# Performance work log

Hardware: AMD Instinct MI355X
Metric: run time of the kernel (lower is better)

## Reference

```python
import jax, jax.numpy as jnp
import numpy as np

IMG = 640
C = 80
K = 10
LB, LC = 7.5, 0.5
ALPHA_COST, BETA_COST = 0.5, 6.0
GAMMA, ALPHA = 2.0, 0.25
EPS = 1e-7
PI = 3.141592653589793


def xywh_to_xyxy(b):
    cx, cy, w, h = b[..., 0], b[..., 1], b[..., 2], b[..., 3]
    return jnp.stack([cx - w * 0.5, cy - h * 0.5, cx + w * 0.5, cy + h * 0.5], axis=-1)


def bbox_iou(box1, box2):
    # box1 [M,4], box2 [N,4] xyxy -> [M,N]
    area1 = jnp.clip(box1[:, 2] - box1[:, 0], 0) * jnp.clip(box1[:, 3] - box1[:, 1], 0)
    area2 = jnp.clip(box2[:, 2] - box2[:, 0], 0) * jnp.clip(box2[:, 3] - box2[:, 1], 0)
    ix1 = jnp.maximum(box1[:, None, 0], box2[None, :, 0])
    iy1 = jnp.maximum(box1[:, None, 1], box2[None, :, 1])
    ix2 = jnp.minimum(box1[:, None, 2], box2[None, :, 2])
    iy2 = jnp.minimum(box1[:, None, 3], box2[None, :, 3])
    inter = jnp.clip(ix2 - ix1, 0) * jnp.clip(iy2 - iy1, 0)
    union = area1[:, None] + area2[None, :] - inter + EPS
    return jnp.clip(inter / union, 0.0, 1.0)


def bbox_ciou(p, t):
    # elementwise [N,4] x [N,4] xyxy -> [N]
    px1, py1, px2, py2 = p[:, 0], p[:, 1], p[:, 2], p[:, 3]
    tx1, ty1, tx2, ty2 = t[:, 0], t[:, 1], t[:, 2], t[:, 3]
    pw = jnp.clip(px2 - px1, EPS)
    ph = jnp.clip(py2 - py1, EPS)
    tw = jnp.clip(tx2 - tx1, EPS)
    th = jnp.clip(ty2 - ty1, EPS)
    inter = jnp.clip(jnp.minimum(px2, tx2) - jnp.maximum(px1, tx1), 0) * \
            jnp.clip(jnp.minimum(py2, ty2) - jnp.maximum(py1, ty1), 0)
    union = pw * ph + tw * th - inter + EPS
    iou = inter / union
    cd = ((px1 + px2) * 0.5 - (tx1 + tx2) * 0.5) ** 2 + ((py1 + py2) * 0.5 - (ty1 + ty2) * 0.5) ** 2
    cw = jnp.maximum(px2, tx2) - jnp.minimum(px1, tx1)
    ch = jnp.maximum(py2, ty2) - jnp.minimum(py1, ty1)
    c2 = cw ** 2 + ch ** 2 + EPS
    v = (4.0 / PI ** 2) * (jnp.arctan(tw / th) - jnp.arctan(pw / ph)) ** 2
    alpha = jax.lax.stop_gradient(v / (v - iou + 1.0 + EPS))
    return iou - cd / c2 - alpha * v


def _decode(p, stride):
    # p: [B, A, S, S, E] -> box [B, A*S*S, 4] (xywh px), cls [B, A*S*S, C]
    B, A, S, _, E = p.shape
    tx, ty, tw, th = p[..., 0], p[..., 1], p[..., 2], p[..., 3]
    gy, gx = jnp.meshgrid(jnp.arange(S, dtype=p.dtype), jnp.arange(S, dtype=p.dtype), indexing='ij')
    gx = gx.reshape(1, 1, S, S)
    gy = gy.reshape(1, 1, S, S)
    px = (jax.nn.sigmoid(tx) * 2.0 - 0.5 + gx) * stride  # center_mode='v8'
    py = (jax.nn.sigmoid(ty) * 2.0 - 0.5 + gy) * stride
    pw = jax.nn.softplus(tw) * stride                      # wh_mode='softplus'
    ph = jax.nn.softplus(th) * stride
    box = jnp.stack([px, py, pw, ph], axis=-1).reshape(B, -1, 4)
    cls = p[..., 4:].reshape(B, -1, C)
    return box, cls


def _per_image(p_box, p_logits, gt, labels):
    # p_box [M,4] xywh, p_logits [M,C], gt [N,4] xyxy, labels [N]
    N = gt.shape[0]
    tcx = (gt[:, 0] + gt[:, 2]) * 0.5
    tcy = (gt[:, 1] + gt[:, 3]) * 0.5
    dist = (p_box[:, 0][:, None] - tcx[None, :]) ** 2 + (p_box[:, 1][:, None] - tcy[None, :]) ** 2  # [M,N]
    _, cand = jax.lax.top_k(-dist.T, K)       # [N,K] nearest anchors per target
    cand = cand.reshape(-1)                    # [N*K] (dups don't change the min)
    cand_box = p_box[cand]
    cand_logits = p_logits[cand]
    cls_score = jax.nn.sigmoid(cand_logits)[:, labels]          # [NK,N]
    iou = bbox_iou(xywh_to_xyxy(cand_box), gt)                  # [NK,N]
    cost = ALPHA_COST * (1.0 - cls_score) + BETA_COST * (1.0 - iou)
    matched = cand[jnp.argmin(cost, axis=0)]                    # [N]
    ciou = bbox_ciou(xywh_to_xyxy(p_box[matched]), gt)
    loss_box = LB * jnp.sum(1.0 - ciou) / N
    tgt = jnp.zeros_like(p_logits).at[matched, labels].set(1.0)  # [M,C]
    x = p_logits
    ce = jnp.maximum(x, 0) - x * tgt + jnp.log1p(jnp.exp(-jnp.abs(x)))
    pr = jax.nn.sigmoid(x)
    p_t = pr * tgt + (1 - pr) * (1 - tgt)
    fl = ce * (1 - p_t) ** GAMMA
    a_t = ALPHA * tgt + (1 - ALPHA) * (1 - tgt)
    loss_cls = LC * jnp.sum(a_t * fl) / N
    return loss_box + loss_cls


def _forward(p0, p1, p2, gt_boxes, labels):
    boxes, logits = [], []
    for p in (p0, p1, p2):
        S = p.shape[2]
        pb, pl = _decode(p, float(IMG) / S)
        boxes.append(pb)
        logits.append(pl)
    flat_boxes = jnp.concatenate(boxes, axis=1)    # [B, 8400, 4]
    flat_logits = jnp.concatenate(logits, axis=1)  # [B, 8400, C]
    per_img = jax.vmap(_per_image)(flat_boxes, flat_logits, gt_boxes, labels)  # [B]
    return jnp.mean(per_img)


def setup_inputs() -> dict:
    key = jax.random.key(0)
    k0, k1, k2, kc, kw, kl = jax.random.split(key, 6)
    B, N = 16, 60
    p0 = jax.random.normal(k0, (B, 1, 80, 80, 84), dtype=jnp.float32)
    p1 = jax.random.normal(k1, (B, 1, 40, 40, 84), dtype=jnp.float32)
    p2 = jax.random.normal(k2, (B, 1, 20, 20, 84), dtype=jnp.float32)
    c = jax.random.uniform(kc, (B, N, 2), minval=64.0, maxval=576.0)
    wh = jax.random.uniform(kw, (B, N, 2), minval=8.0, maxval=128.0)
    gt_boxes = jnp.concatenate([c - wh * 0.5, c + wh * 0.5], axis=-1).astype(jnp.float32)
    labels = jax.random.randint(kl, (B, N), 0, 80, dtype=jnp.int32)
    return {"p0": p0, "p1": p1, "p2": p2, "gt_boxes": gt_boxes, "labels": labels}


def reference(p0, p1, p2, gt_boxes, labels):
    return _forward(p0, p1, p2, gt_boxes, labels)
```

## Files before the change

kernel.cpp:

```cpp
#include <hip/hip_runtime.h>
#include <cfloat>
#include <math.h>

#define NB   16
#define NGT  60
#define NA   8400
#define KNN  10
#define NCAND (NGT*KNN)
#define EPSF 1e-7f
#define PIF  3.14159265358979f
#define FOCAL_BLOCKS 2048

#define LOG2E 1.44269504088896341f
#define LN2   0.69314718055994531f

__device__ __forceinline__ float fexp2(float x){ return __builtin_amdgcn_exp2f(x); }
__device__ __forceinline__ float flog2(float x){ return __builtin_amdgcn_logf(x); }
__device__ __forceinline__ float frcp (float x){ return __builtin_amdgcn_rcpf(x); }

__device__ __forceinline__ float fsigm(float x){
  return frcp(1.0f + fexp2(-x*LOG2E));
}
__device__ __forceinline__ float fsoftplus(float x){
  float u = fexp2(-fabsf(x)*LOG2E);
  return fmaxf(x,0.f) + LN2*flog2(1.0f + u);
}
__device__ __forceinline__ float fbg(float x){
  float u = fexp2(fminf(-x*LOG2E, 126.0f));
  float t = frcp(1.0f + u);
  return (x + LN2*flog2(1.0f + u)) * t * t;
}

template<int S, int BASE, int STRIDE_I>
__device__ __forceinline__ void do_vec(const float* __restrict__ p, unsigned vloc,
                                       float4* __restrict__ boxes, float& sum){
  unsigned s = vloc*4u;
  float4 x4 = *(const float4*)(p + s);
  if ((s % 84u) == 0u){
    unsigned row   = s / 84u;
    unsigned img   = row / (unsigned)(S*S);
    unsigned local = row - img*(unsigned)(S*S);
    unsigned i = local / (unsigned)S, j = local - i*(unsigned)S;
    const float stf = (float)STRIDE_I;
    float px = (fsigm(x4.x)*2.f - 0.5f + (float)j)*stf;
    float py = (fsigm(x4.y)*2.f - 0.5f + (float)i)*stf;
    float pw = fsoftplus(x4.z)*stf;
    float ph = fsoftplus(x4.w)*stf;
    boxes[(size_t)img*NA + BASE + local] = make_float4(px,py,pw,ph);
  } else {
    sum += fbg(x4.x) + fbg(x4.y) + fbg(x4.z) + fbg(x4.w);
  }
}

__global__ __launch_bounds__(256) void fused_decode_focal(const float* __restrict__ p0,
                                                          const float* __restrict__ p1,
                                                          const float* __restrict__ p2,
                                                          float4* __restrict__ boxes,
                                                          float* __restrict__ fsum){
  const unsigned nv0 = NB*6400u*84u/4u;
  const unsigned nv1 = NB*1600u*84u/4u;
  const unsigned nv2 = NB*400u*84u/4u;
  const unsigned total = nv0+nv1+nv2;
  __shared__ float sbuf[4];
  float sum = 0.f;
  unsigned stride = gridDim.x*blockDim.x;
  for (unsigned v = blockIdx.x*blockDim.x + threadIdx.x; v < total; v += stride){
    if (v < nv0)          do_vec<80,    0,  8>(p0, v,          boxes, sum);
    else if (v < nv0+nv1) do_vec<40, 6400, 16>(p1, v-nv0,      boxes, sum);
    else                  do_vec<20, 8000, 32>(p2, v-nv0-nv1,  boxes, sum);
  }
  sum *= 0.75f;
  #pragma unroll
  for (int off=32; off>0; off>>=1) sum += __shfl_xor(sum, off);
  int wid = threadIdx.x >> 6;
  if ((threadIdx.x & 63) == 0) sbuf[wid] = sum;
  __syncthreads();
  if (threadIdx.x == 0) fsum[blockIdx.x] = sbuf[0]+sbuf[1]+sbuf[2]+sbuf[3];
}

__device__ __forceinline__ const float* anchor_base(const float* p0,const float* p1,const float* p2,int img,int a){
  if (a < 6400) return p0 + (size_t)(img*6400 + a)*84;
  if (a < 8000) return p1 + (size_t)(img*1600 + (a-6400))*84;
  return p2 + (size_t)(img*400 + (a-8000))*84;
}

__global__ __launch_bounds__(256) void topk_kernel(const float4* __restrict__ boxes,
                                                   const float* __restrict__ gt,
                                                   int* __restrict__ cand){
  int wid  = threadIdx.x >> 6;
  int lane = threadIdx.x & 63;
  int pair = blockIdx.x*4 + wid;
  int img = pair / NGT, g = pair - img*NGT;
  const float* gb = gt + (size_t)(img*NGT + g)*4;
  float tcx = (gb[0]+gb[2])*0.5f, tcy = (gb[1]+gb[3])*0.5f;

  int jx0 = (int)(tcx * 0.125f),   iy0 = (int)(tcy * 0.125f);
  int jx1 = (int)(tcx * 0.0625f),  iy1 = (int)(tcy * 0.0625f);
  int jx2 = (int)(tcx * 0.03125f), iy2 = (int)(tcy * 0.03125f);

  const float4* bb = boxes + (size_t)img*NA;

  float d0=FLT_MAX,d1=FLT_MAX,d2=FLT_MAX,d3=FLT_MAX;
  int   a0,a1,a2,a3;
  #pragma unroll
  for (int s=0; s<4; s++){
    int c = lane + 64*s;
    float dd = FLT_MAX; int aa = 9000000 + c;
    int i, j, S, base, valid = 1;
    if (c < 169)      { int r=c/13,  q=c-13*r;           i=iy0-6+r; j=jx0-6+q; S=80; base=0; }
    else if (c < 218) { int t=c-169; int r=t/7, q=t-7*r; i=iy1-3+r; j=jx1-3+q; S=40; base=6400; }
    else if (c < 243) { int t=c-218; int r=t/5, q=t-5*r; i=iy2-2+r; j=jx2-2+q; S=20; base=8000; }
    else { valid = 0; i=j=0; S=1; base=0; }
    if (valid && i>=0 && i<S && j>=0 && j<S){
      int anchor = base + i*S + j;
      float4 b = bb[anchor];
      float dx=b.x-tcx, dy=b.y-tcy;
      dd = dx*dx + dy*dy;
      aa = anchor;
    }
    if (s==0){ d0=dd; a0=aa; } else if (s==1){ d1=dd; a1=aa; }
    else if (s==2){ d2=dd; a2=aa; } else { d3=dd; a3=aa; }
  }

  for (int r=0; r<KNN; r++){
    float v = d0; int anc = a0;
    if (d1 < v || (d1==v && a1<anc)){ v=d1; anc=a1; }
    if (d2 < v || (d2==v && a2<anc)){ v=d2; anc=a2; }
    if (d3 < v || (d3==v && a3<anc)){ v=d3; anc=a3; }
    #pragma unroll
    for (int off=32; off>0; off>>=1){
      float v2 = __shfl_xor(v, off);
      int  A2 = __shfl_xor(anc, off);
      if (v2 < v || (v2==v && A2<anc)){ v=v2; anc=A2; }
    }
    if (a0==anc) d0=FLT_MAX;
    if (a1==anc) d1=FLT_MAX;
    if (a2==anc) d2=FLT_MAX;
    if (a3==anc) d3=FLT_MAX;
    if (lane == 0) cand[(size_t)pair*KNN + r] = anc;
  }
}

__global__ __launch_bounds__(256) void match_kernel(const float4* __restrict__ boxes,
                                                    const int* __restrict__ cand,
                                                    const float* __restrict__ gt,
                                                    const int* __restrict__ labels,
                                                    const float* __restrict__ p0,
                                                    const float* __restrict__ p1,
                                                    const float* __restrict__ p2,
                                                    int* __restrict__ matched){
  int pair = blockIdx.x;
  int img = pair / NGT, j = pair - img*NGT;
  int tid = threadIdx.x;
  int wid = tid >> 6, lane = tid & 63;
  const float* gb = gt + (size_t)(img*NGT + j)*4;
  float gx=gb[0], gy=gb[1], gz=gb[2], gw=gb[3];
  float a2 = fmaxf(gz-gx,0.f)*fmaxf(gw-gy,0.f);
  int lab = labels[img*NGT + j];

  const int* ci = cand + (size_t)img*NCAND;
  float best = FLT_MAX; int bslot = 1<<30; int banchor = -1;
  for (int c=tid; c<NCAND; c+=256){
    int a = ci[c];
    float4 b = boxes[(size_t)img*NA + a];
    float bx1=b.x-b.z*0.5f, by1=b.y-b.w*0.5f, bx2=b.x+b.z*0.5f, by2=b.y+b.w*0.5f;
    float a1 = fmaxf(bx2-bx1,0.f)*fmaxf(by2-by1,0.f);
    float ix1=fmaxf(bx1,gx), iy1=fmaxf(by1,gy);
    float ix2=fminf(bx2,gz), iy2=fminf(by2,gw);
    float inter = fmaxf(ix2-ix1,0.f)*fmaxf(iy2-iy1,0.f);
    float uni = a1 + a2 - inter + EPSF;
    float iou = fminf(fmaxf(inter/uni,0.f),1.f);
    float lg = anchor_base(p0,p1,p2,img,a)[4+lab];
    float cost = 0.5f*(1.f - fsigm(lg)) + 6.f*(1.f - iou);
    if (cost < best){ best=cost; bslot=c; banchor=a; }
  }
  #pragma unroll
  for (int off=32; off>0; off>>=1){
    float v2 = __shfl_xor(best, off);
    int  s2 = __shfl_xor(bslot, off);
    int  a2s= __shfl_xor(banchor, off);
    if (v2 < best || (v2==best && s2<bslot)){ best=v2; bslot=s2; banchor=a2s; }
  }
  __shared__ float bc[4]; __shared__ int bs[4], ba[4];
  if (lane == 0){ bc[wid]=best; bs[wid]=bslot; ba[wid]=banchor; }
  __syncthreads();
  if (tid == 0){
    float v=bc[0]; int s=bs[0]; int a=ba[0];
    #pragma unroll
    for (int k=1;k<4;k++){
      if (bc[k] < v || (bc[k]==v && bs[k]<s)){ v=bc[k]; s=bs[k]; a=ba[k]; }
    }
    matched[img*NGT + j] = a;
  }
}

__global__ __launch_bounds__(1024) void tail_kernel(const float4* __restrict__ boxes,
                                                    const int* __restrict__ matched_g,
                                                    const float* __restrict__ gt,
                                                    const int* __restrict__ labels,
                                                    const float* __restrict__ p0,
                                                    const float* __restrict__ p1,
                                                    const float* __restrict__ p2,
                                                    const float* __restrict__ fsum,
                                                    float* __restrict__ out){
  int tid = threadIdx.x;
  int wid = tid >> 6;
  int lane = tid & 63;
  __shared__ int sm[NB][NGT];
  __shared__ int sl[NB][NGT];
  __shared__ float wb[NB], wc[NB], wf[NB];
  if (lane < NGT){
    sm[wid][lane] = matched_g[wid*NGT + lane];
    sl[wid][lane] = labels[wid*NGT + lane];
  }
  __syncthreads();

  int img = wid;
  float local_box = 0.f, local_corr = 0.f;
  if (lane < NGT){
    int j = lane;
    int m = sm[img][j];
    float4 pb = boxes[(size_t)img*NA + m];
    float px1=pb.x-pb.z*0.5f, py1=pb.y-pb.w*0.5f, px2=pb.x+pb.z*0.5f, py2=pb.y+pb.w*0.5f;
    const float* gb = gt + (size_t)(img*NGT + j)*4;
    float gx=gb[0], gy=gb[1], gz=gb[2], gw=gb[3];
    float pw=fmaxf(px2-px1,EPSF), ph=fmaxf(py2-py1,EPSF);
    float tw=fmaxf(gz-gx,EPSF),  th=fmaxf(gw-gy,EPSF);
    float inter = fmaxf(fminf(px2,gz)-fmaxf(px1,gx),0.f)*fmaxf(fminf(py2,gw)-fmaxf(py1,gy),0.f);
    float uni = pw*ph + tw*th - inter + EPSF;
    float iou = inter/uni;
    float dcx = (px1+px2)*0.5f - (gx+gz)*0.5f;
    float dcy = (py1+py2)*0.5f - (gy+gw)*0.5f;
    float cd = dcx*dcx + dcy*dcy;
    float cw = fmaxf(px2,gz) - fminf(px1,gx);
    float ch = fmaxf(py2,gw) - fminf(py1,gy);
    float c2 = cw*cw + ch*ch + EPSF;
    float dv = atanf(tw/th) - atanf(pw/ph);
    float v  = (4.f/(PIF*PIF))*dv*dv;
    float alpha = v/(v - iou + 1.f + EPSF);
    float ciou = iou - cd/c2 - alpha*v;
    local_box = 1.f - ciou;

    int lab = sl[img][j];
    bool dup = false;
    for (int j2=0; j2<j; j2++)
      if (sm[img][j2]==m && sl[img][j2]==lab){ dup=true; break; }
    if (!dup){
      float x = anchor_base(p0,p1,p2,img,m)[4+lab];
      float s  = fsigm(x);
      float u  = fexp2(-fabsf(x)*LOG2E);
      float lt = LN2*flog2(1.0f + u);
      float sp_pos = fmaxf(-x,0.f) + lt;
      float sp_neg = fmaxf( x,0.f) + lt;
      local_corr = 0.25f*sp_pos*(1.f-s)*(1.f-s) - 0.75f*sp_neg*s*s;
    }
  }
  float local_f = fsum[tid] + fsum[tid + 1024];
  #pragma unroll
  for (int off=32; off>0; off>>=1){
    local_box  += __shfl_xor(local_box,  off);
    local_corr += __shfl_xor(local_corr, off);
    local_f    += __shfl_xor(local_f,    off);
  }
  if (lane == 0){ wb[wid]=local_box; wc[wid]=local_corr; wf[wid]=local_f; }
  __syncthreads();
  if (tid == 0){
    float sb=0.f, sc=0.f, sf=0.f;
    #pragma unroll
    for (int k=0;k<NB;k++){ sb+=wb[k]; sc+=wc[k]; sf+=wf[k]; }
    out[0] = (7.5f*sb + 0.5f*(sf + sc)) / (60.f*16.f);
  }
}

extern "C" void kernel_launch(void* const* d_in, const int* in_sizes, int n_in,
                              void* d_out, int out_size, void* d_ws, size_t ws_size,
                              hipStream_t stream){
  const float* p0 = (const float*)d_in[0];
  const float* p1 = (const float*)d_in[1];
  const float* p2 = (const float*)d_in[2];
  const float* gt = (const float*)d_in[3];
  const int* labels = (const int*)d_in[4];
  float* out = (float*)d_out;

  float4* boxes   = (float4*)d_ws;
  int*    cand    = (int*)((char*)d_ws + (size_t)NB*NA*sizeof(float4));
  int*    matched = (int*)((char*)cand + (size_t)NB*NCAND*sizeof(int));
  float*  fsum    = (float*)((char*)matched + (size_t)NB*NGT*sizeof(int));

  fused_decode_focal<<<FOCAL_BLOCKS, 256, 0, stream>>>(p0, p1, p2, boxes, fsum);
  topk_kernel<<<NB*NGT/4, 256, 0, stream>>>(boxes, gt, cand);
  match_kernel<<<NB*NGT, 256, 0, stream>>>(boxes, cand, gt, labels, p0, p1, p2, matched);
  tail_kernel<<<1, 1024, 0, stream>>>(boxes, matched, gt, labels, p0, p1, p2, fsum, out);
}
```

Measured before the change: 47.68 us.

## Fuse match and tail kernels via last-block atomic; split focal vs decode work

Merges the match kernel and the single-block tail kernel into one launch, where the last block to finish (detected by an atomic counter reset in the decode kernel) performs the final CIoU/correction/focal reduction. Also reorganizes the decode/focal loop so focal-only float4 vectors are enumerated directly (skipping the box columns) and box rows are decoded in a separate index range, removing the per-vector modulo branch divergence. This removes one kernel launch and the divergent branch, at the cost of an atomic plus threadfence per block and a serialized tail on one 256-thread block.

```diff
diff --git a/kernel.cpp b/kernel.cpp
--- a/kernel.cpp
+++ b/kernel.cpp
@@ -11,6 +11,13 @@
 #define PIF  3.14159265358979f
 #define FOCAL_BLOCKS 2048
 
+#define NV0   2150400u
+#define NV1    537600u
+#define NV2    134400u
+#define NVTOT 2822400u
+#define NROWS  134400u
+#define FOCAL_COUNT 2688000u
+
 #define LOG2E 1.44269504088896341f
 #define LN2   0.69314718055994531f
 
@@ -32,42 +39,46 @@
 }
 
 template<int S, int BASE, int STRIDE_I>
-__device__ __forceinline__ void do_vec(const float* __restrict__ p, unsigned vloc,
-                                       float4* __restrict__ boxes, float& sum){
-  unsigned s = vloc*4u;
-  float4 x4 = *(const float4*)(p + s);
-  if ((s % 84u) == 0u){
-    unsigned row   = s / 84u;
-    unsigned img   = row / (unsigned)(S*S);
-    unsigned local = row - img*(unsigned)(S*S);
-    unsigned i = local / (unsigned)S, j = local - i*(unsigned)S;
-    const float stf = (float)STRIDE_I;
-    float px = (fsigm(x4.x)*2.f - 0.5f + (float)j)*stf;
-    float py = (fsigm(x4.y)*2.f - 0.5f + (float)i)*stf;
-    float pw = fsoftplus(x4.z)*stf;
-    float ph = fsoftplus(x4.w)*stf;
-    boxes[(size_t)img*NA + BASE + local] = make_float4(px,py,pw,ph);
-  } else {
-    sum += fbg(x4.x) + fbg(x4.y) + fbg(x4.z) + fbg(x4.w);
-  }
+__device__ __forceinline__ void decode_row(const float* __restrict__ p, unsigned row,
+                                           float4* __restrict__ boxes){
+  unsigned img   = row / (unsigned)(S*S);
+  unsigned local = row - img*(unsigned)(S*S);
+  unsigned i = local / (unsigned)S, j = local - i*(unsigned)S;
+  float4 x4 = *(const float4*)(p + (size_t)row*84u);
+  const float stf = (float)STRIDE_I;
+  float px = (fsigm(x4.x)*2.f - 0.5f + (float)j)*stf;
+  float py = (fsigm(x4.y)*2.f - 0.5f + (float)i)*stf;
+  float pw = fsoftplus(x4.z)*stf;
+  float ph = fsoftplus(x4.w)*stf;
+  boxes[(size_t)img*NA + BASE + local] = make_float4(px,py,pw,ph);
 }
 
 __global__ __launch_bounds__(256) void fused_decode_focal(const float* __restrict__ p0,
                                                           const float* __restrict__ p1,
                                                           const float* __restrict__ p2,
                                                           float4* __restrict__ boxes,
-                                                          float* __restrict__ fsum){
-  const unsigned nv0 = NB*6400u*84u/4u;
-  const unsigned nv1 = NB*1600u*84u/4u;
-  const unsigned nv2 = NB*400u*84u/4u;
-  const unsigned total = nv0+nv1+nv2;
+                                                          float* __restrict__ fsum,
+                                                          int* __restrict__ done){
+  if (blockIdx.x == 0 && threadIdx.x == 0) *done = 0;
   __shared__ float sbuf[4];
   float sum = 0.f;
   unsigned stride = gridDim.x*blockDim.x;
-  for (unsigned v = blockIdx.x*blockDim.x + threadIdx.x; v < total; v += stride){
-    if (v < nv0)          do_vec<80,    0,  8>(p0, v,          boxes, sum);
-    else if (v < nv0+nv1) do_vec<40, 6400, 16>(p1, v-nv0,      boxes, sum);
-    else                  do_vec<20, 8000, 32>(p2, v-nv0-nv1,  boxes, sum);
+  for (unsigned u = blockIdx.x*blockDim.x + threadIdx.x; u < NVTOT; u += stride){
+    if (u < FOCAL_COUNT){
+      unsigned g = u / 20u;
+      unsigned v = 21u*g + (u - 20u*g) + 1u;
+      const float* p; unsigned vloc;
+      if (v < NV0)           { p=p0; vloc = v; }
+      else if (v < NV0+NV1)  { p=p1; vloc = v - NV0; }
+      else                   { p=p2; vloc = v - (NV0+NV1); }
+      float4 x4 = *(const float4*)(p + (size_t)vloc*4u);
+      sum += fbg(x4.x) + fbg(x4.y) + fbg(x4.z) + fbg(x4.w);
+    } else {
+      unsigned row = u - FOCAL_COUNT;
+      if (row < 102400u)      decode_row<80,    0,  8>(p0, row,           boxes);
+      else if (row < 128000u) decode_row<40, 6400, 16>(p1, row - 102400u, boxes);
+      else                    decode_row<20, 8000, 32>(p2, row - 128000u, boxes);
+    }
   }
   sum *= 0.75f;
   #pragma unroll
@@ -141,133 +152,138 @@
   }
 }
 
-__global__ __launch_bounds__(256) void match_kernel(const float4* __restrict__ boxes,
-                                                    const int* __restrict__ cand,
-                                                    const float* __restrict__ gt,
-                                                    const int* __restrict__ labels,
-                                                    const float* __restrict__ p0,
-                                                    const float* __restrict__ p1,
-                                                    const float* __restrict__ p2,
-                                                    int* __restrict__ matched){
+__global__ __launch_bounds__(256) void match_tail_kernel(const float4* __restrict__ boxes,
+                                                         const int* __restrict__ cand,
+                                                         const float* __restrict__ gt,
+                                                         const int* __restrict__ labels,
+                                                         const float* __restrict__ p0,
+                                                         const float* __restrict__ p1,
+                                                         const float* __restrict__ p2,
+                                                         int* __restrict__ matched,
+                                                         const float* __restrict__ fsum,
+                                                         int* __restrict__ done,
+                                                         float* __restrict__ out){
   int pair = blockIdx.x;
   int img = pair / NGT, j = pair - img*NGT;
   int tid = threadIdx.x;
   int wid = tid >> 6, lane = tid & 63;
-  const float* gb = gt + (size_t)(img*NGT + j)*4;
-  float gx=gb[0], gy=gb[1], gz=gb[2], gw=gb[3];
-  float a2 = fmaxf(gz-gx,0.f)*fmaxf(gw-gy,0.f);
-  int lab = labels[img*NGT + j];
-
-  const int* ci = cand + (size_t)img*NCAND;
-  float best = FLT_MAX; int bslot = 1<<30; int banchor = -1;
-  for (int c=tid; c<NCAND; c+=256){
-    int a = ci[c];
-    float4 b = boxes[(size_t)img*NA + a];
-    float bx1=b.x-b.z*0.5f, by1=b.y-b.w*0.5f, bx2=b.x+b.z*0.5f, by2=b.y+b.w*0.5f;
-    float a1 = fmaxf(bx2-bx1,0.f)*fmaxf(by2-by1,0.f);
-    float ix1=fmaxf(bx1,gx), iy1=fmaxf(by1,gy);
-    float ix2=fminf(bx2,gz), iy2=fminf(by2,gw);
-    float inter = fmaxf(ix2-ix1,0.f)*fmaxf(iy2-iy1,0.f);
-    float uni = a1 + a2 - inter + EPSF;
-    float iou = fminf(fmaxf(inter/uni,0.f),1.f);
-    float lg = anchor_base(p0,p1,p2,img,a)[4+lab];
-    float cost = 0.5f*(1.f - fsigm(lg)) + 6.f*(1.f - iou);
-    if (cost < best){ best=cost; bslot=c; banchor=a; }
-  }
-  #pragma unroll
-  for (int off=32; off>0; off>>=1){
-    float v2 = __shfl_xor(best, off);
-    int  s2 = __shfl_xor(bslot, off);
-    int  a2s= __shfl_xor(banchor, off);
-    if (v2 < best || (v2==best && s2<bslot)){ best=v2; bslot=s2; banchor=a2s; }
-  }
-  __shared__ float bc[4]; __shared__ int bs[4], ba[4];
-  if (lane == 0){ bc[wid]=best; bs[wid]=bslot; ba[wid]=banchor; }
-  __syncthreads();
-  if (tid == 0){
-    float v=bc[0]; int s=bs[0]; int a=ba[0];
-    #pragma unroll
-    for (int k=1;k<4;k++){
-      if (bc[k] < v || (bc[k]==v && bs[k]<s)){ v=bc[k]; s=bs[k]; a=ba[k]; }
-    }
-    matched[img*NGT + j] = a;
-  }
-}
-
-__global__ __launch_bounds__(1024) void tail_kernel(const float4* __restrict__ boxes,
-                                                    const int* __restrict__ matched_g,
-                                                    const float* __restrict__ gt,
-                                                    const int* __restrict__ labels,
-                                                    const float* __restrict__ p0,
-                                                    const float* __restrict__ p1,
-                                                    const float* __restrict__ p2,
-                                                    const float* __restrict__ fsum,
-                                                    float* __restrict__ out){
-  int tid = threadIdx.x;
-  int wid = tid >> 6;
-  int lane = tid & 63;
-  __shared__ int sm[NB][NGT];
-  __shared__ int sl[NB][NGT];
-  __shared__ float wb[NB], wc[NB], wf[NB];
-  if (lane < NGT){
-    sm[wid][lane] = matched_g[wid*NGT + lane];
-    sl[wid][lane] = labels[wid*NGT + lane];
-  }
-  __syncthreads();
-
-  int img = wid;
-  float local_box = 0.f, local_corr = 0.f;
-  if (lane < NGT){
-    int j = lane;
-    int m = sm[img][j];
-    float4 pb = boxes[(size_t)img*NA + m];
-    float px1=pb.x-pb.z*0.5f, py1=pb.y-pb.w*0.5f, px2=pb.x+pb.z*0.5f, py2=pb.y+pb.w*0.5f;
+  {
     const float* gb = gt + (size_t)(img*NGT + j)*4;
     float gx=gb[0], gy=gb[1], gz=gb[2], gw=gb[3];
-    float pw=fmaxf(px2-px1,EPSF), ph=fmaxf(py2-py1,EPSF);
-    float tw=fmaxf(gz-gx,EPSF),  th=fmaxf(gw-gy,EPSF);
-    float inter = fmaxf(fminf(px2,gz)-fmaxf(px1,gx),0.f)*fmaxf(fminf(py2,gw)-fmaxf(py1,gy),0.f);
-    float uni = pw*ph + tw*th - inter + EPSF;
-    float iou = inter/uni;
-    float dcx = (px1+px2)*0.5f - (gx+gz)*0.5f;
-    float dcy = (py1+py2)*0.5f - (gy+gw)*0.5f;
-    float cd = dcx*dcx + dcy*dcy;
-    float cw = fmaxf(px2,gz) - fminf(px1,gx);
-    float ch = fmaxf(py2,gw) - fminf(py1,gy);
-    float c2 = cw*cw + ch*ch + EPSF;
-    float dv = atanf(tw/th) - atanf(pw/ph);
-    float v  = (4.f/(PIF*PIF))*dv*dv;
-    float alpha = v/(v - iou + 1.f + EPSF);
-    float ciou = iou - cd/c2 - alpha*v;
-    local_box = 1.f - ciou;
-
-    int lab = sl[img][j];
-    bool dup = false;
-    for (int j2=0; j2<j; j2++)
-      if (sm[img][j2]==m && sl[img][j2]==lab){ dup=true; break; }
-    if (!dup){
-      float x = anchor_base(p0,p1,p2,img,m)[4+lab];
-      float s  = fsigm(x);
-      float u  = fexp2(-fabsf(x)*LOG2E);
-      float lt = LN2*flog2(1.0f + u);
-      float sp_pos = fmaxf(-x,0.f) + lt;
-      float sp_neg = fmaxf( x,0.f) + lt;
-      local_corr = 0.25f*sp_pos*(1.f-s)*(1.f-s) - 0.75f*sp_neg*s*s;
-    }
-  }
-  float local_f = fsum[tid] + fsum[tid + 1024];
+    float a2 = fmaxf(gz-gx,0.f)*fmaxf(gw-gy,0.f);
+    int lab = labels[img*NGT + j];
+
+    const int* ci = cand + (size_t)img*NCAND;
+    float best = FLT_MAX; int bslot = 1<<30; int banchor = -1;
+    for (int c=tid; c<NCAND; c+=256){
+      int a = ci[c];
+      float4 b = boxes[(size_t)img*NA + a];
+      float bx1=b.x-b.z*0.5f, by1=b.y-b.w*0.5f, bx2=b.x+b.z*0.5f, by2=b.y+b.w*0.5f;
+      float a1 = fmaxf(bx2-bx1,0.f)*fmaxf(by2-by1,0.f);
+      float ix1=fmaxf(bx1,gx), iy1=fmaxf(by1,gy);
+      float ix2=fminf(bx2,gz), iy2=fminf(by2,gw);
+      float inter = fmaxf(ix2-ix1,0.f)*fmaxf(iy2-iy1,0.f);
+      float uni = a1 + a2 - inter + EPSF;
+      float iou = fminf(fmaxf(inter/uni,0.f),1.f);
+      float lg = anchor_base(p0,p1,p2,img,a)[4+lab];
+      float cost = 0.5f*(1.f - fsigm(lg)) + 6.f*(1.f - iou);
+      if (cost < best){ best=cost; bslot=c; banchor=a; }
+    }
+    #pragma unroll
+    for (int off=32; off>0; off>>=1){
+      float v2 = __shfl_xor(best, off);
+      int  s2 = __shfl_xor(bslot, off);
+      int  a2s= __shfl_xor(banchor, off);
+      if (v2 < best || (v2==best && s2<bslot)){ best=v2; bslot=s2; banchor=a2s; }
+    }
+    __shared__ float bc[4]; __shared__ int bs[4], ba[4];
+    if (lane == 0){ bc[wid]=best; bs[wid]=bslot; ba[wid]=banchor; }
+    __syncthreads();
+    if (tid == 0){
+      float v=bc[0]; int s=bs[0]; int a=ba[0];
+      #pragma unroll
+      for (int k=1;k<4;k++){
+        if (bc[k] < v || (bc[k]==v && bs[k]<s)){ v=bc[k]; s=bs[k]; a=ba[k]; }
+      }
+      matched[img*NGT + j] = a;
+    }
+  }
+
+  __shared__ int lastflag;
+  if (tid == 0){
+    __threadfence();
+    int old = atomicAdd(done, 1);
+    lastflag = (old == NB*NGT - 1);
+  }
+  __syncthreads();
+  if (!lastflag) return;
+  __threadfence();
+
+  __shared__ int sm[NB*NGT];
+  __shared__ int sl[NB*NGT];
+  for (int t=tid; t<NB*NGT; t+=256){ sm[t]=matched[t]; sl[t]=labels[t]; }
+  __syncthreads();
+
+  float local_box = 0.f, local_corr = 0.f;
+  #pragma unroll
+  for (int q=0; q<4; q++){
+    int im = wid*4 + q;
+    if (lane < NGT){
+      int jj = lane;
+      int m = sm[im*NGT + jj];
+      float4 pb = boxes[(size_t)im*NA + m];
+      float px1=pb.x-pb.z*0.5f, py1=pb.y-pb.w*0.5f, px2=pb.x+pb.z*0.5f, py2=pb.y+pb.w*0.5f;
+      const float* gb = gt + (size_t)(im*NGT + jj)*4;
+      float gx=gb[0], gy=gb[1], gz=gb[2], gw=gb[3];
+      float pw=fmaxf(px2-px1,EPSF), ph=fmaxf(py2-py1,EPSF);
+      float tw=fmaxf(gz-gx,EPSF),  th=fmaxf(gw-gy,EPSF);
+      float inter = fmaxf(fminf(px2,gz)-fmaxf(px1,gx),0.f)*fmaxf(fminf(py2,gw)-fmaxf(py1,gy),0.f);
+      float uni = pw*ph + tw*th - inter + EPSF;
+      float iou = inter/uni;
+      float dcx = (px1+px2)*0.5f - (gx+gz)*0.5f;
+      float dcy = (py1+py2)*0.5f - (gy+gw)*0.5f;
+      float cd = dcx*dcx + dcy*dcy;
+      float cw = fmaxf(px2,gz) - fminf(px1,gx);
+      float ch = fmaxf(py2,gw) - fminf(py1,gy);
+      float c2 = cw*cw + ch*ch + EPSF;
+      float dv = atanf(tw/th) - atanf(pw/ph);
+      float v  = (4.f/(PIF*PIF))*dv*dv;
+      float alpha = v/(v - iou + 1.f + EPSF);
+      float ciou = iou - cd/c2 - alpha*v;
+      local_box += 1.f - ciou;
+
+      int lab = sl[im*NGT + jj];
+      bool dup = false;
+      for (int j2=0; j2<jj; j2++)
+        if (sm[im*NGT + j2]==m && sl[im*NGT + j2]==lab){ dup=true; break; }
+      if (!dup){
+        float x = anchor_base(p0,p1,p2,im,m)[4+lab];
+        float s  = fsigm(x);
+        float u  = fexp2(-fabsf(x)*LOG2E);
+        float lt = LN2*flog2(1.0f + u);
+        float sp_pos = fmaxf(-x,0.f) + lt;
+        float sp_neg = fmaxf( x,0.f) + lt;
+        local_corr += 0.25f*sp_pos*(1.f-s)*(1.f-s) - 0.75f*sp_neg*s*s;
+      }
+    }
+  }
+  float local_f = 0.f;
+  #pragma unroll
+  for (int k=0; k<FOCAL_BLOCKS/256; k++) local_f += fsum[tid + 256*k];
+
   #pragma unroll
   for (int off=32; off>0; off>>=1){
     local_box  += __shfl_xor(local_box,  off);
     local_corr += __shfl_xor(local_corr, off);
     local_f    += __shfl_xor(local_f,    off);
   }
+  __shared__ float wb[4], wc[4], wf[4];
   if (lane == 0){ wb[wid]=local_box; wc[wid]=local_corr; wf[wid]=local_f; }
   __syncthreads();
   if (tid == 0){
     float sb=0.f, sc=0.f, sf=0.f;
     #pragma unroll
-    for (int k=0;k<NB;k++){ sb+=wb[k]; sc+=wc[k]; sf+=wf[k]; }
+    for (int k=0;k<4;k++){ sb+=wb[k]; sc+=wc[k]; sf+=wf[k]; }
     out[0] = (7.5f*sb + 0.5f*(sf + sc)) / (60.f*16.f);
   }
 }
@@ -286,9 +302,10 @@
   int*    cand    = (int*)((char*)d_ws + (size_t)NB*NA*sizeof(float4));
   int*    matched = (int*)((char*)cand + (size_t)NB*NCAND*sizeof(int));
   float*  fsum    = (float*)((char*)matched + (size_t)NB*NGT*sizeof(int));
-
-  fused_decode_focal<<<FOCAL_BLOCKS, 256, 0, stream>>>(p0, p1, p2, boxes, fsum);
+  int*    done    = (int*)((char*)fsum + FOCAL_BLOCKS*sizeof(float));
+
+  fused_decode_focal<<<FOCAL_BLOCKS, 256, 0, stream>>>(p0, p1, p2, boxes, fsum, done);
   topk_kernel<<<NB*NGT/4, 256, 0, stream>>>(boxes, gt, cand);
-  match_kernel<<<NB*NGT, 256, 0, stream>>>(boxes, cand, gt, labels, p0, p1, p2, matched);
-  tail_kernel<<<1, 1024, 0, stream>>>(boxes, matched, gt, labels, p0, p1, p2, fsum, out);
-}
+  match_tail_kernel<<<NB*NGT, 256, 0, stream>>>(boxes, cand, gt, labels, p0, p1, p2,
+                                                matched, fsum, done, out);
+}
```

Result: slower. 81.95 us (+71.9%).
